# Kernel optimization log

Measured on AMD Instinct MI355X. Metric: run time of the kernel, lower is better.

Reference implementation:

```python
import jax, jax.numpy as jnp
import numpy as np

B, S, D, H, E, K = 4, 1024, 1024, 4096, 8, 2
CAPACITY_FACTOR = 2.0
T = B * S
CAP = int(T * CAPACITY_FACTOR * K / E)  # 2048


def setup_inputs() -> dict:
    key = jax.random.key(0)
    ks = jax.random.split(key, 6)
    std = 0.02
    return {
        "x": jax.random.normal(ks[0], (B, S, D), dtype=jnp.float32),
        "router_w": jax.random.normal(ks[1], (E, D), dtype=jnp.float32) * std,
        "w1": jax.random.normal(ks[2], (E, D, H), dtype=jnp.float32) * std,
        "b1": jnp.zeros((E, H), dtype=jnp.float32),
        "w2": jax.random.normal(ks[3], (E, H, D), dtype=jnp.float32) * std,
        "b2": jnp.zeros((E, D), dtype=jnp.float32),
    }


def reference(x, router_w, w1, b1, w2, b2):
    # Router (eval mode: no logit noise, no dropout)
    logits = jnp.einsum("bsd,ed->bse", x, router_w)            # [B,S,E]
    probs = jax.nn.softmax(logits, axis=-1)
    topk_p, topk_i = jax.lax.top_k(probs, K)                   # [B,S,K]
    gates = topk_p / jnp.sum(topk_p, axis=-1, keepdims=True)

    xt = x.reshape(T, D)                                        # tokens
    eidx = topk_i.reshape(T * K)                                # expert per slot
    g = gates.reshape(T * K)
    tok = jnp.arange(T * K) // K                                # token id per slot

    # position of each slot within its expert (first-come-first-served capacity)
    oh = jax.nn.one_hot(eidx, E, dtype=jnp.int32)               # [T*K, E]
    pos = jnp.sum((jnp.cumsum(oh, axis=0) - 1) * oh, axis=1)    # [T*K]
    keep = pos < CAP
    pos_c = jnp.where(keep, pos, CAP)                           # overflow -> padding row

    # dispatch: gather tokens into per-expert buffers [E, CAP, D]
    buf = jnp.zeros((E, CAP + 1, D), x.dtype).at[eidx, pos_c].set(xt[tok])
    inp = buf[:, :CAP]

    # per-expert FFN (exact-erf GELU matches torch nn.GELU default)
    h = jax.nn.gelu(jnp.einsum("ecd,edh->ech", inp, w1) + b1[:, None, :],
                    approximate=False)
    out_e = jnp.einsum("ech,eho->eco", h, w2) + b2[:, None, :]  # [E,CAP,D]

    # combine: gather back to slots, weight by gates, sum over k per token
    gathered = out_e[eidx, jnp.minimum(pos_c, CAP - 1)]         # [T*K, D]
    wslot = g * keep.astype(x.dtype)
    out = (gathered * wslot[:, None]).reshape(T, K, D).sum(axis=1).reshape(B, S, D)

    # load-balancing loss
    router_prob_per_expert = probs.mean(axis=(0, 1))            # [E]
    expert_usage = oh.sum(axis=0).astype(x.dtype) / (T * K)
    lb_loss = jnp.sum(router_prob_per_expert * expert_usage) * E
    return out, lb_loss
```

## Files before the change

kernel.cpp:

```cpp
#include <hip/hip_runtime.h>
#include <cstdint>
#include <cstddef>

#define TDIM 4096
#define DDIM 1024
#define HDIM 4096
#define EDIM 8
#define CAPD 2048
#define NSLOT 8192
#define NROUTERBLK 1024

typedef _Float16 f16;
typedef _Float16 f16x2 __attribute__((ext_vector_type(2)));
typedef _Float16 f16x4 __attribute__((ext_vector_type(4)));
typedef _Float16 f16x8 __attribute__((ext_vector_type(8)));
typedef float f32x4 __attribute__((ext_vector_type(4)));

__device__ __forceinline__ void gload16(const void* g, void* l) {
  __builtin_amdgcn_global_load_lds(
      (const __attribute__((address_space(1))) unsigned int*)g,
      (__attribute__((address_space(3))) unsigned int*)l, 16, 0, 0);
}

__device__ __forceinline__ float gelu_fast(float x) {
  float y = 1.5957691216057308f * (x + 0.044715f * x * x * x);
  y = fminf(y, 60.f);
  float e = __expf(y);
  return x * e * __builtin_amdgcn_rcpf(e + 1.f);
}

#define MEMFENCE asm volatile("" ::: "memory")
#define VMCNT(n) asm volatile("s_waitcnt vmcnt(" #n ")" ::: "memory")
#define BAR_ENTER MEMFENCE; __builtin_amdgcn_s_barrier(); \
  asm volatile("s_waitcnt lgkmcnt(0)" ::: "memory")
#define BAR_EXIT __builtin_amdgcn_s_barrier(); MEMFENCE

__global__ __launch_bounds__(256)
void transpose_cvt(const float* __restrict__ src, f16* __restrict__ dst, int R, int C) {
  __shared__ float tile[64][65];
  const int e = blockIdx.z;
  const int c0 = blockIdx.x * 64, r0 = blockIdx.y * 64;
  const int tid = threadIdx.x;
  const float* s = src + (size_t)e * R * C;
  f16* d = dst + (size_t)e * R * C;
  #pragma unroll
  for (int p = 0; p < 4; ++p) {
    const int row = p * 16 + (tid >> 4);
    const int col = (tid & 15) * 4;
    float4 v = *(const float4*)(s + (size_t)(r0 + row) * C + c0 + col);
    tile[row][col] = v.x; tile[row][col + 1] = v.y;
    tile[row][col + 2] = v.z; tile[row][col + 3] = v.w;
  }
  __syncthreads();
  #pragma unroll
  for (int p = 0; p < 4; ++p) {
    const int crow = p * 16 + (tid >> 4);
    const int q = (tid & 15) * 4;
    f16x4 o;
    #pragma unroll
    for (int j = 0; j < 4; ++j) o[j] = (f16)tile[q + j][crow];
    *(f16x4*)(d + (size_t)(c0 + crow) * R + r0 + q) = o;
  }
}

__global__ void router_k(const float* __restrict__ x, const float* __restrict__ rw,
                         int* __restrict__ eidx, float* __restrict__ gates,
                         float* __restrict__ bps) {
  __shared__ float lrw[EDIM * DDIM];
  __shared__ float wps[4][EDIM];
  const int tid = threadIdx.x, lane = tid & 63, wv = tid >> 6;
  for (int i = tid; i < EDIM * DDIM; i += 256) lrw[i] = rw[i];
  __syncthreads();
  const int t = blockIdx.x * 4 + wv;
  float acc[EDIM];
  #pragma unroll
  for (int e = 0; e < EDIM; ++e) acc[e] = 0.f;
  const float* xr = x + (size_t)t * DDIM;
  #pragma unroll
  for (int j = 0; j < DDIM / 64; ++j) {
    float xv = xr[j * 64 + lane];
    #pragma unroll
    for (int e = 0; e < EDIM; ++e) acc[e] += xv * lrw[e * DDIM + j * 64 + lane];
  }
  #pragma unroll
  for (int off = 32; off >= 1; off >>= 1) {
    #pragma unroll
    for (int e = 0; e < EDIM; ++e) acc[e] += __shfl_xor(acc[e], off);
  }
  float mx = acc[0];
  #pragma unroll
  for (int e = 1; e < EDIM; ++e) mx = fmaxf(mx, acc[e]);
  float p[EDIM], s = 0.f;
  #pragma unroll
  for (int e = 0; e < EDIM; ++e) { p[e] = expf(acc[e] - mx); s += p[e]; }
  float inv = 1.f / s;
  #pragma unroll
  for (int e = 0; e < EDIM; ++e) p[e] *= inv;
  int i1 = 0; float p1 = p[0];
  #pragma unroll
  for (int e = 1; e < EDIM; ++e) if (p[e] > p1) { p1 = p[e]; i1 = e; }
  int i2 = (i1 == 0) ? 1 : 0; float p2 = p[i2];
  #pragma unroll
  for (int e = 0; e < EDIM; ++e) if (e != i1 && p[e] > p2) { p2 = p[e]; i2 = e; }
  float gs = 1.f / (p1 + p2);
  if (lane == 0) {
    eidx[2 * t] = i1; eidx[2 * t + 1] = i2;
    gates[2 * t] = p1 * gs; gates[2 * t + 1] = p2 * gs;
    #pragma unroll
    for (int e = 0; e < EDIM; ++e) wps[wv][e] = p[e];
  }
  __syncthreads();
  if (tid < EDIM)
    bps[blockIdx.x * EDIM + tid] = wps[0][tid] + wps[1][tid] + wps[2][tid] + wps[3][tid];
}

__global__ void count_k(const int* __restrict__ eidx, int* __restrict__ cc) {
  __shared__ int h[EDIM];
  const int tid = threadIdx.x;
  if (tid < EDIM) h[tid] = 0;
  __syncthreads();
  atomicAdd(&h[eidx[blockIdx.x * 256 + tid]], 1);
  __syncthreads();
  if (tid < EDIM) cc[blockIdx.x * EDIM + tid] = h[tid];
}

__global__ void scan_k(const int* __restrict__ cc, const float* __restrict__ bps,
                       int* __restrict__ cb, int* __restrict__ counts,
                       int* __restrict__ rowsNeeded, float* __restrict__ lb_out) {
  __shared__ float red[32][EDIM];
  __shared__ int cnt_s[EDIM];
  const int tid = threadIdx.x;
  const int e = tid & 7, g = tid >> 3;
  float s = 0.f;
  for (int j = 0; j < 32; ++j) s += bps[(g + 32 * j) * EDIM + e];
  red[g][e] = s;
  __syncthreads();
  for (int st = 16; st >= 1; st >>= 1) {
    if (g < st) red[g][e] += red[g + st][e];
    __syncthreads();
  }
  if (tid < EDIM) {
    int base = 0;
    for (int c = 0; c < 32; ++c) { cb[c * EDIM + tid] = base; base += cc[c * EDIM + tid]; }
    counts[tid] = base;
    rowsNeeded[tid] = base < CAPD ? base : CAPD;
    cnt_s[tid] = base;
  }
  __syncthreads();
  if (tid == 0) {
    float lb = 0.f;
    for (int ee = 0; ee < EDIM; ++ee)
      lb += (red[0][ee] / (float)TDIM) * ((float)cnt_s[ee] / (float)NSLOT);
    lb_out[0] = lb * (float)EDIM;
  }
}

__global__ void pos_k(const int* __restrict__ eidx, const float* __restrict__ gates,
                      const int* __restrict__ cb, int* __restrict__ posa,
                      float* __restrict__ wslot) {
  __shared__ int wcnt[4][EDIM];
  const int tid = threadIdx.x, lane = tid & 63, wv = tid >> 6;
  const int slot = blockIdx.x * 256 + tid;
  const int e = eidx[slot];
  const unsigned long long below = (1ull << lane) - 1ull;
  int wavepos = 0;
  #pragma unroll
  for (int ee = 0; ee < EDIM; ++ee) {
    unsigned long long m = __ballot(e == ee);
    if (lane == 0) wcnt[wv][ee] = __popcll(m);
    if (e == ee) wavepos = __popcll(m & below);
  }
  __syncthreads();
  int off = 0;
  for (int w = 0; w < wv; ++w) off += wcnt[w][e];
  const int pos = cb[blockIdx.x * EDIM + e] + off + wavepos;
  posa[slot] = pos;
  wslot[slot] = (pos < CAPD) ? gates[slot] : 0.f;
}

__global__ void scatter_k(const float* __restrict__ x, const int* __restrict__ eidx,
                          const int* __restrict__ posa, f16* __restrict__ buf) {
  const int s = blockIdx.x, lane = threadIdx.x;
  const int p = posa[s];
  if (p >= CAPD) return;
  const int e = eidx[s], tok = s >> 1;
  const float4* src = (const float4*)(x + (size_t)tok * DDIM);
  f16x4* dst = (f16x4*)(buf + ((size_t)e * CAPD + p) * DDIM);
  #pragma unroll
  for (int j = 0; j < DDIM / 4 / 64; ++j) {
    float4 v = src[j * 64 + lane];
    f16x4 o; o.x = (f16)v.x; o.y = (f16)v.y; o.z = (f16)v.z; o.w = (f16)v.w;
    dst[j * 64 + lane] = o;
  }
}

#define LDA(bb, MH) do { \
    const char* base_ = smem + (bb) * 65536 + wr * 16384; \
    _Pragma("unroll") for (int m_ = 0; m_ < 4; ++m_) \
    _Pragma("unroll") for (int k_ = 0; k_ < 2; ++k_) { \
      const int rh_ = (MH) * 64 + m_ * 16 + ro; \
      af[m_][k_] = *(const f16x8*)(base_ + rh_ * 128 + ((k_ * 64 + ko0b) ^ ((rh_ & 7) << 4))); \
    } } while (0)

#define LDB(bb, NH, BF) do { \
    const char* base_ = smem + (bb) * 65536 + (2 + (wc >> 1)) * 16384; \
    _Pragma("unroll") for (int n_ = 0; n_ < 2; ++n_) \
    _Pragma("unroll") for (int k_ = 0; k_ < 2; ++k_) { \
      const int rh_ = (wc & 1) * 64 + (NH) * 32 + n_ * 16 + ro; \
      (BF)[n_][k_] = *(const f16x8*)(base_ + rh_ * 128 + ((k_ * 64 + ko0b) ^ ((rh_ & 7) << 4))); \
    } } while (0)

#define MM16(AM, AN, BF) do { \
    __builtin_amdgcn_s_setprio(1); \
    _Pragma("unroll") for (int m_ = 0; m_ < 4; ++m_) \
    _Pragma("unroll") for (int n_ = 0; n_ < 2; ++n_) \
    _Pragma("unroll") for (int k_ = 0; k_ < 2; ++k_) \
      acc[(AM) + m_][(AN) + n_] = __builtin_amdgcn_mfma_f32_16x16x32_f16( \
          af[m_][k_], (BF)[n_][k_], acc[(AM) + m_][(AN) + n_], 0, 0, 0); \
    __builtin_amdgcn_s_setprio(0); \
  } while (0)

#define STAGE(bb, hh2, g) do { \
    const f16* s_ = (((hh2) < 2) ? (aBase + (size_t)((hh2) * 128) * LD) \
                                 : (bBase + (size_t)(((hh2) - 2) * 128) * LD)) \
                    + (size_t)row0 * LD + (g) * 64 + sw0; \
    char* d_ = smem + (bb) * 65536 + (hh2) * 16384 + wv * 1024; \
    gload16(s_, d_); \
    gload16(s_ + (size_t)64 * LD, d_ + 8192); \
  } while (0)

template<int KLEN, int LD, int N, int GELU, int NT, int NKS>
__global__ __launch_bounds__(512, 1)
void gemm256p(const f16* __restrict__ A, const f16* __restrict__ Bt,
              const float* __restrict__ bias, f16* __restrict__ C, size_t pstride,
              const int* __restrict__ rowsNeeded) {
  constexpr int NI = KLEN / 128;
  __shared__ __align__(128) char smem[131072];
  const int wg = blockIdx.x;
  const int e = wg & 7;
  const int r = wg >> 3;
  const int nt = r % NT;
  const int ks = (r / NT) % NKS;
  const int mt = r / (NT * NKS);
  if (mt * 256 >= rowsNeeded[e]) return;
  const int tid = threadIdx.x, lane = tid & 63, wv = tid >> 6;
  const int wr = wv >> 2, wc = wv & 3;
  const int ro = lane & 15, q4 = (lane >> 4) * 4;
  const int ko0b = (lane >> 4) * 16;
  const f16* aBase = A + ((size_t)e * CAPD + (size_t)mt * 256) * LD + (size_t)ks * KLEN;
  const f16* bBase = Bt + ((size_t)e * N + (size_t)nt * 256) * LD + (size_t)ks * KLEN;
  const int row0 = tid >> 3;
  const int sw0 = ((tid & 7) ^ (row0 & 7)) * 8;

  f16x8 af[4][2], bf0[2][2], bf1[2][2];
  f32x4 acc[8][4];
  #pragma unroll
  for (int m = 0; m < 8; ++m)
    #pragma unroll
    for (int n = 0; n < 4; ++n) acc[m][n] = (f32x4){0.f, 0.f, 0.f, 0.f};

  STAGE(0, 2, 0); STAGE(0, 3, 0); STAGE(0, 0, 0); STAGE(0, 1, 0);
  STAGE(1, 2, 1); STAGE(1, 3, 1);
  VMCNT(4);
  __builtin_amdgcn_s_barrier(); MEMFENCE;

  #pragma unroll 1
  for (int i = 0; i < NI - 1; ++i) {
    const int g0 = 2 * i;
    LDA(0, 0); LDB(0, 0, bf0);
    STAGE(1, 0, g0 + 1);
    BAR_ENTER; MM16(0, 0, bf0); BAR_EXIT;
    LDB(0, 1, bf1);
    STAGE(1, 1, g0 + 1);
    BAR_ENTER; MM16(0, 2, bf1); BAR_EXIT;
    LDA(0, 1);
    STAGE(0, 2, g0 + 2);
    BAR_ENTER; MM16(4, 2, bf1); BAR_EXIT;
    STAGE(0, 3, g0 + 2);
    VMCNT(4);
    BAR_ENTER; MM16(4, 0, bf0); BAR_EXIT;
    LDA(1, 0); LDB(1, 0, bf0);
    STAGE(0, 0, g0 + 2);
    BAR_ENTER; MM16(0, 0, bf0); BAR_EXIT;
    LDB(1, 1, bf1);
    STAGE(0, 1, g0 + 2);
    BAR_ENTER; MM16(0, 2, bf1); BAR_EXIT;
    LDA(1, 1);
    STAGE(1, 2, g0 + 3);
    BAR_ENTER; MM16(4, 2, bf1); BAR_EXIT;
    STAGE(1, 3, g0 + 3);
    VMCNT(4);
    BAR_ENTER; MM16(4, 0, bf0); BAR_EXIT;
  }
  {
    LDA(0, 0); LDB(0, 0, bf0);
    STAGE(1, 0, 2 * NI - 1);
    BAR_ENTER; MM16(0, 0, bf0); BAR_EXIT;
    LDB(0, 1, bf1);
    STAGE(1, 1, 2 * NI - 1);
    BAR_ENTER; MM16(0, 2, bf1); BAR_EXIT;
    LDA(0, 1);
    BAR_ENTER; MM16(4, 2, bf1); BAR_EXIT;
    VMCNT(0);
    BAR_ENTER; MM16(4, 0, bf0); BAR_EXIT;
    LDA(1, 0); LDB(1, 0, bf0);
    BAR_ENTER; MM16(0, 0, bf0); BAR_EXIT;
    LDB(1, 1, bf1);
    BAR_ENTER; MM16(0, 2, bf1); BAR_EXIT;
    LDA(1, 1);
    BAR_ENTER; MM16(4, 2, bf1); BAR_EXIT;
    BAR_ENTER; MM16(4, 0, bf0); BAR_EXIT;
  }

  float bv[4];
  #pragma unroll
  for (int n = 0; n < 4; ++n)
    bv[n] = (ks == 0) ? bias[e * N + nt * 256 + wc * 64 + n * 16 + ro] : 0.f;
  f16* Ct = (f16*)(smem + wv * 16384);
  #pragma unroll
  for (int m = 0; m < 8; ++m)
    #pragma unroll
    for (int n = 0; n < 4; ++n)
      #pragma unroll
      for (int i = 0; i < 4; ++i) {
        const int row = m * 16 + q4 + i;
        float v = acc[m][n][i] + bv[n];
        if (GELU) v = gelu_fast(v);
        *(f16*)((char*)Ct + row * 128 + ((((n * 16 + ro) * 2)) ^ (((row >> 2) & 3) << 5))) = (f16)v;
      }
  asm volatile("s_waitcnt lgkmcnt(0)" ::: "memory");
  f16* Cp = C + (size_t)ks * pstride;
  const size_t crow0 = (size_t)e * CAPD + mt * 256 + wr * 128;
  const int ccol0 = nt * 256 + wc * 64;
  #pragma unroll
  for (int j = 0; j < 16; ++j) {
    const int idx = j * 64 + lane;
    const int rr = idx >> 3, c2 = (idx & 7) * 16;
    f16x8 v = *(const f16x8*)((const char*)Ct + rr * 128 + (c2 ^ (((rr >> 2) & 3) << 5)));
    *(f16x8*)(Cp + (crow0 + rr) * N + ccol0 + (idx & 7) * 8) = v;
  }
}

__global__ void combine_k(const f16* __restrict__ pA, const f16* __restrict__ pB,
                          const int* __restrict__ eidx, const int* __restrict__ posa,
                          const float* __restrict__ wslot, float* __restrict__ out) {
  const int t = blockIdx.x, tid = threadIdx.x;
  const int s0 = 2 * t, s1 = 2 * t + 1;
  const int e0 = eidx[s0], e1 = eidx[s1];
  int p0 = posa[s0]; p0 = p0 < CAPD - 1 ? p0 : CAPD - 1;
  int p1 = posa[s1]; p1 = p1 < CAPD - 1 ? p1 : CAPD - 1;
  const float g0 = wslot[s0], g1 = wslot[s1];
  const size_t o0 = ((size_t)e0 * CAPD + p0) * DDIM;
  const size_t o1 = ((size_t)e1 * CAPD + p1) * DDIM;
  const f16x2* r0a = (const f16x2*)(pA + o0);
  const f16x2* r0b = (const f16x2*)(pB + o0);
  const f16x2* r1a = (const f16x2*)(pA + o1);
  const f16x2* r1b = (const f16x2*)(pB + o1);
  float2* o = (float2*)(out + (size_t)t * DDIM);
  #pragma unroll
  for (int j = tid; j < DDIM / 2; j += 256) {
    f16x2 a0 = r0a[j], a1 = r0b[j], b0 = r1a[j], b1 = r1b[j];
    o[j] = make_float2(
        g0 * ((float)a0.x + (float)a1.x) + g1 * ((float)b0.x + (float)b1.x),
        g0 * ((float)a0.y + (float)a1.y) + g1 * ((float)b0.y + (float)b1.y));
  }
}

extern "C" void kernel_launch(void* const* d_in, const int* in_sizes, int n_in,
                              void* d_out, int out_size, void* d_ws, size_t ws_size,
                              hipStream_t stream) {
  (void)in_sizes; (void)n_in; (void)out_size; (void)ws_size;
  const float* x  = (const float*)d_in[0];
  const float* rw = (const float*)d_in[1];
  const float* w1 = (const float*)d_in[2];
  const float* b1 = (const float*)d_in[3];
  const float* w2 = (const float*)d_in[4];
  const float* b2 = (const float*)d_in[5];
  float* out = (float*)d_out;

  char* ws = (char*)d_ws;
  size_t off = 0;
  auto alloc = [&](size_t b) { void* p = ws + off; off += (b + 255) & ~(size_t)255; return p; };
  f16* w1t   = (f16*)alloc((size_t)EDIM * DDIM * HDIM * 2);
  f16* w2t   = (f16*)alloc((size_t)EDIM * DDIM * HDIM * 2);
  f16* buf   = (f16*)alloc((size_t)EDIM * CAPD * DDIM * 2);
  f16* hbuf  = (f16*)alloc((size_t)EDIM * CAPD * HDIM * 2);
  const size_t PSTRIDE = (size_t)EDIM * CAPD * DDIM;
  f16* outeA = (f16*)alloc(PSTRIDE * 2);
  f16* outeB = (f16*)alloc(PSTRIDE * 2);
  int*   eidx   = (int*)alloc(NSLOT * 4);
  int*   posa   = (int*)alloc(NSLOT * 4);
  float* gatesA = (float*)alloc(NSLOT * 4);
  float* wslotA = (float*)alloc(NSLOT * 4);
  int*   cc     = (int*)alloc(32 * EDIM * 4);
  int*   cb     = (int*)alloc(32 * EDIM * 4);
  int*   counts = (int*)alloc(EDIM * 4);
  int*   rowsN  = (int*)alloc(EDIM * 4);
  float* bps    = (float*)alloc(NROUTERBLK * EDIM * 4);
  (void)outeB;

  transpose_cvt<<<dim3(HDIM / 64, DDIM / 64, EDIM), 256, 0, stream>>>(w1, w1t, DDIM, HDIM);
  transpose_cvt<<<dim3(DDIM / 64, HDIM / 64, EDIM), 256, 0, stream>>>(w2, w2t, HDIM, DDIM);

  router_k<<<NROUTERBLK, 256, 0, stream>>>(x, rw, eidx, gatesA, bps);
  count_k<<<32, 256, 0, stream>>>(eidx, cc);
  scan_k<<<1, 256, 0, stream>>>(cc, bps, cb, counts, rowsN, out + (size_t)TDIM * DDIM);
  pos_k<<<32, 256, 0, stream>>>(eidx, gatesA, cb, posa, wslotA);
  scatter_k<<<NSLOT, 64, 0, stream>>>(x, eidx, posa, buf);

  gemm256p<DDIM, DDIM, HDIM, 1, 16, 1><<<1024, 512, 0, stream>>>(
      buf, w1t, b1, hbuf, 0, rowsN);

  gemm256p<HDIM / 2, HDIM, DDIM, 0, 4, 2><<<512, 512, 0, stream>>>(
      hbuf, w2t, b2, outeA, PSTRIDE, rowsN);

  combine_k<<<TDIM, 256, 0, stream>>>(outeA, outeA + PSTRIDE, eidx, posa, wslotA, out);
}
```

Measured before the change: 330.6 us.

## Double-buffer LDS fragment registers to overlap ds_reads with MFMA in GEMM loop

Restructures the GEMM main loop so each phase issues the LDS fragment loads for the next MFMA group while the current group runs. It uses two A-fragment register sets and two B0 sets, and replaces the two-barrier enter/exit pattern with a single barrier per phase. The waits are tightened to vmcnt(2). This is meant to hide LDS read latency behind MFMA work and halve barrier count. The cost is higher register pressure and more subtle ordering requirements between LDS reads and the async global-to-LDS stages overwriting the buffers.

```diff
diff --git a/kernel.cpp b/kernel.cpp
--- a/kernel.cpp
+++ b/kernel.cpp
@@ -31,9 +31,7 @@
 
 #define MEMFENCE asm volatile("" ::: "memory")
 #define VMCNT(n) asm volatile("s_waitcnt vmcnt(" #n ")" ::: "memory")
-#define BAR_ENTER MEMFENCE; __builtin_amdgcn_s_barrier(); \
-  asm volatile("s_waitcnt lgkmcnt(0)" ::: "memory")
-#define BAR_EXIT __builtin_amdgcn_s_barrier(); MEMFENCE
+#define BAR do { MEMFENCE; __builtin_amdgcn_s_barrier(); MEMFENCE; } while (0)
 
 __global__ __launch_bounds__(256)
 void transpose_cvt(const float* __restrict__ src, f16* __restrict__ dst, int R, int C) {
@@ -194,15 +192,15 @@
   }
 }
 
-#define LDA(bb, MH) do { \
+#define LDA_(bb, MH, AF) do { \
     const char* base_ = smem + (bb) * 65536 + wr * 16384; \
     _Pragma("unroll") for (int m_ = 0; m_ < 4; ++m_) \
     _Pragma("unroll") for (int k_ = 0; k_ < 2; ++k_) { \
       const int rh_ = (MH) * 64 + m_ * 16 + ro; \
-      af[m_][k_] = *(const f16x8*)(base_ + rh_ * 128 + ((k_ * 64 + ko0b) ^ ((rh_ & 7) << 4))); \
+      (AF)[m_][k_] = *(const f16x8*)(base_ + rh_ * 128 + ((k_ * 64 + ko0b) ^ ((rh_ & 7) << 4))); \
     } } while (0)
 
-#define LDB(bb, NH, BF) do { \
+#define LDB_(bb, NH, BF) do { \
     const char* base_ = smem + (bb) * 65536 + (2 + (wc >> 1)) * 16384; \
     _Pragma("unroll") for (int n_ = 0; n_ < 2; ++n_) \
     _Pragma("unroll") for (int k_ = 0; k_ < 2; ++k_) { \
@@ -210,13 +208,13 @@
       (BF)[n_][k_] = *(const f16x8*)(base_ + rh_ * 128 + ((k_ * 64 + ko0b) ^ ((rh_ & 7) << 4))); \
     } } while (0)
 
-#define MM16(AM, AN, BF) do { \
+#define MM16_(AM, AN, AF, BF) do { \
     __builtin_amdgcn_s_setprio(1); \
     _Pragma("unroll") for (int m_ = 0; m_ < 4; ++m_) \
     _Pragma("unroll") for (int n_ = 0; n_ < 2; ++n_) \
     _Pragma("unroll") for (int k_ = 0; k_ < 2; ++k_) \
       acc[(AM) + m_][(AN) + n_] = __builtin_amdgcn_mfma_f32_16x16x32_f16( \
-          af[m_][k_], (BF)[n_][k_], acc[(AM) + m_][(AN) + n_], 0, 0, 0); \
+          (AF)[m_][k_], (BF)[n_][k_], acc[(AM) + m_][(AN) + n_], 0, 0, 0); \
     __builtin_amdgcn_s_setprio(0); \
   } while (0)
 
@@ -252,7 +250,7 @@
   const int row0 = tid >> 3;
   const int sw0 = ((tid & 7) ^ (row0 & 7)) * 8;
 
-  f16x8 af[4][2], bf0[2][2], bf1[2][2];
+  f16x8 af_a[4][2], af_b[4][2], bf0_a[2][2], bf0_b[2][2], bf1[2][2];
   f32x4 acc[8][4];
   #pragma unroll
   for (int m = 0; m < 8; ++m)
@@ -262,54 +260,31 @@
   STAGE(0, 2, 0); STAGE(0, 3, 0); STAGE(0, 0, 0); STAGE(0, 1, 0);
   STAGE(1, 2, 1); STAGE(1, 3, 1);
   VMCNT(4);
-  __builtin_amdgcn_s_barrier(); MEMFENCE;
+  BAR;
+  LDA_(0, 0, af_a); LDB_(0, 0, bf0_a);
 
   #pragma unroll 1
   for (int i = 0; i < NI - 1; ++i) {
     const int g0 = 2 * i;
-    LDA(0, 0); LDB(0, 0, bf0);
-    STAGE(1, 0, g0 + 1);
-    BAR_ENTER; MM16(0, 0, bf0); BAR_EXIT;
-    LDB(0, 1, bf1);
-    STAGE(1, 1, g0 + 1);
-    BAR_ENTER; MM16(0, 2, bf1); BAR_EXIT;
-    LDA(0, 1);
-    STAGE(0, 2, g0 + 2);
-    BAR_ENTER; MM16(4, 2, bf1); BAR_EXIT;
-    STAGE(0, 3, g0 + 2);
-    VMCNT(4);
-    BAR_ENTER; MM16(4, 0, bf0); BAR_EXIT;
-    LDA(1, 0); LDB(1, 0, bf0);
-    STAGE(0, 0, g0 + 2);
-    BAR_ENTER; MM16(0, 0, bf0); BAR_EXIT;
-    LDB(1, 1, bf1);
-    STAGE(0, 1, g0 + 2);
-    BAR_ENTER; MM16(0, 2, bf1); BAR_EXIT;
-    LDA(1, 1);
-    STAGE(1, 2, g0 + 3);
-    BAR_ENTER; MM16(4, 2, bf1); BAR_EXIT;
-    STAGE(1, 3, g0 + 3);
-    VMCNT(4);
-    BAR_ENTER; MM16(4, 0, bf0); BAR_EXIT;
+    STAGE(1, 0, g0 + 1); LDB_(0, 1, bf1);          MM16_(0, 0, af_a, bf0_a); BAR;
+    STAGE(1, 1, g0 + 1); LDA_(0, 1, af_b);         MM16_(0, 2, af_a, bf1);   BAR;
+    STAGE(0, 2, g0 + 2);                           MM16_(4, 2, af_b, bf1);   VMCNT(2); BAR;
+    STAGE(0, 3, g0 + 2); LDA_(1, 0, af_a); LDB_(1, 0, bf0_b); MM16_(4, 0, af_b, bf0_a); BAR;
+    STAGE(0, 0, g0 + 2); LDB_(1, 1, bf1);          MM16_(0, 0, af_a, bf0_b); BAR;
+    STAGE(0, 1, g0 + 2); LDA_(1, 1, af_b);         MM16_(0, 2, af_a, bf1);   BAR;
+    STAGE(1, 2, g0 + 3);                           MM16_(4, 2, af_b, bf1);   VMCNT(2); BAR;
+    STAGE(1, 3, g0 + 3); LDA_(0, 0, af_a); LDB_(0, 0, bf0_a); MM16_(4, 0, af_b, bf0_b); BAR;
   }
   {
-    LDA(0, 0); LDB(0, 0, bf0);
-    STAGE(1, 0, 2 * NI - 1);
-    BAR_ENTER; MM16(0, 0, bf0); BAR_EXIT;
-    LDB(0, 1, bf1);
-    STAGE(1, 1, 2 * NI - 1);
-    BAR_ENTER; MM16(0, 2, bf1); BAR_EXIT;
-    LDA(0, 1);
-    BAR_ENTER; MM16(4, 2, bf1); BAR_EXIT;
-    VMCNT(0);
-    BAR_ENTER; MM16(4, 0, bf0); BAR_EXIT;
-    LDA(1, 0); LDB(1, 0, bf0);
-    BAR_ENTER; MM16(0, 0, bf0); BAR_EXIT;
-    LDB(1, 1, bf1);
-    BAR_ENTER; MM16(0, 2, bf1); BAR_EXIT;
-    LDA(1, 1);
-    BAR_ENTER; MM16(4, 2, bf1); BAR_EXIT;
-    BAR_ENTER; MM16(4, 0, bf0); BAR_EXIT;
+    const int g1 = 2 * NI - 1;
+    STAGE(1, 0, g1); LDB_(0, 1, bf1);  MM16_(0, 0, af_a, bf0_a); BAR;
+    STAGE(1, 1, g1); LDA_(0, 1, af_b); MM16_(0, 2, af_a, bf1);   BAR;
+    MM16_(4, 2, af_b, bf1); VMCNT(0); BAR;
+    LDA_(1, 0, af_a); LDB_(1, 0, bf0_b); MM16_(4, 0, af_b, bf0_a); BAR;
+    LDB_(1, 1, bf1);  MM16_(0, 0, af_a, bf0_b); BAR;
+    LDA_(1, 1, af_b); MM16_(0, 2, af_a, bf1);   BAR;
+    MM16_(4, 2, af_b, bf1); BAR;
+    MM16_(4, 0, af_b, bf0_b); BAR;
   }
 
   float bv[4];
```

After: 380.0 us. +14.9%, slower.
